# Performance work log

Hardware: AMD Instinct MI355X
Metric: run time of the kernel (lower is better)

## Reference

```python
import jax, jax.numpy as jnp
import numpy as np

B, S, D, H = 4, 2048, 1024, 16
DK = D // H

def setup_inputs() -> dict:
    key = jax.random.key(0)
    ks = jax.random.split(key, 5)
    x = jax.random.normal(ks[0], (B, S, D), dtype=jnp.float32)
    scale = 1.0 / np.sqrt(D)
    Wq = jax.random.normal(ks[1], (D, D), dtype=jnp.float32) * scale
    Wk = jax.random.normal(ks[2], (D, D), dtype=jnp.float32) * scale
    Wv = jax.random.normal(ks[3], (D, D), dtype=jnp.float32) * scale
    Wo = jax.random.normal(ks[4], (D, D), dtype=jnp.float32) * scale
    return {"x": x, "Wq": Wq, "Wk": Wk, "Wv": Wv, "Wo": Wo}

def reference(x, Wq, Wk, Wv, Wo):
    # F.linear: y = x @ W.T  (weights stored torch-style [out, in])
    q = jnp.einsum('bsd,ed->bse', x, Wq).reshape(B, S, H, DK).transpose(0, 2, 1, 3)
    k = jnp.einsum('bsd,ed->bse', x, Wk).reshape(B, S, H, DK).transpose(0, 2, 1, 3)
    v = jnp.einsum('bsd,ed->bse', x, Wv).reshape(B, S, H, DK).transpose(0, 2, 1, 3)
    scores = jnp.einsum('bhqd,bhkd->bhqk', q, k) / jnp.sqrt(jnp.float32(DK))
    attn = jax.nn.softmax(scores, axis=-1)  # dropout p=0.0 -> identity
    out = jnp.einsum('bhqk,bhkd->bhqd', attn, v)
    out = out.transpose(0, 2, 1, 3).reshape(B, S, D)
    return jnp.einsum('bsd,ed->bse', out, Wo)
```

## Files before the change

### kernel.cpp

```cpp
#include <hip/hip_runtime.h>
#include <hip/hip_bf16.h>

#define B_ 4
#define S_ 2048
#define D_ 1024
#define H_ 16
#define DK_ 64

typedef __attribute__((ext_vector_type(8))) short short8;
typedef __attribute__((ext_vector_type(4))) float floatx4;
typedef __attribute__((ext_vector_type(16))) float floatx16;
typedef __attribute__((ext_vector_type(4))) unsigned int uint4v;

#define QSCL 0.1803368801111204f

static __device__ __forceinline__ unsigned short f2bf(float f) {
    unsigned int u = __float_as_uint(f);
    u += 0x7fffu + ((u >> 16) & 1u);
    return (unsigned short)(u >> 16);
}

static __device__ __forceinline__ unsigned int pack2bf_perm(float a, float b) {
    unsigned int u0 = __float_as_uint(a) + 0x8000u;
    unsigned int u1 = __float_as_uint(b) + 0x8000u;
    return __builtin_amdgcn_perm(u1, u0, 0x07060302u);
}

static __device__ __forceinline__ unsigned int pack2bf(float a, float b) {
    return (unsigned int)f2bf(a) | ((unsigned int)f2bf(b) << 16);
}

#define PLSWAP(a, b) asm volatile("v_permlane32_swap_b32 %0, %1" : "+v"(a), "+v"(b))

struct CastAll {
    const float* x;
    const float* w[4];
    unsigned short* xd;
    unsigned short* wd[4];
};

__global__ void cast_all_kernel(CastAll a) {
    int i = blockIdx.x * blockDim.x + threadIdx.x;
    const float* s;
    unsigned short* d;
    int j;
    if (i < 2097152) {
        s = a.x; d = a.xd; j = i;
    } else {
        int k = i - 2097152;
        int w = k >> 18;
        j = k & 262143;
        s = a.w[w]; d = a.wd[w];
    }
    float4 v = ((const float4*)s)[j];
    ushort4 o;
    o.x = f2bf(v.x); o.y = f2bf(v.y); o.z = f2bf(v.z); o.w = f2bf(v.w);
    ((ushort4*)d)[j] = o;
}

template <typename OutT, bool VT2>
__global__ __launch_bounds__(256) void gemm_bt(
    const unsigned short* __restrict__ A,
    const unsigned short* __restrict__ W0,
    const unsigned short* __restrict__ W1,
    const unsigned short* __restrict__ W2,
    OutT* __restrict__ C0, OutT* __restrict__ C1, OutT* __restrict__ C2,
    int M, int N, int K)
{
    __shared__ __align__(16) unsigned short At[128 * 64];
    __shared__ __align__(16) unsigned short Bt[128 * 64];

    const unsigned short* W = (blockIdx.z == 0) ? W0 : ((blockIdx.z == 1) ? W1 : W2);
    OutT* C = (blockIdx.z == 0) ? C0 : ((blockIdx.z == 1) ? C1 : C2);

    const int m0 = blockIdx.x * 128;
    const int n0 = blockIdx.y * 128;
    const int wv = threadIdx.x >> 6;
    const int ln = threadIdx.x & 63;
    const int l31 = ln & 31;
    const int half = ln >> 5;
    const int wm = (wv >> 1) * 64;
    const int wn = (wv & 1) * 64;

    floatx16 acc[2][2];
#pragma unroll
    for (int mt = 0; mt < 2; mt++)
#pragma unroll
        for (int nt = 0; nt < 2; nt++)
#pragma unroll
            for (int e = 0; e < 16; e++) acc[mt][nt][e] = 0.f;

    const int lr = ln >> 3;
    const int lc = (((ln & 7) ^ lr) * 8);
    const int sw = (l31 & 7);

    for (int k0 = 0; k0 < K; k0 += 64) {
        __syncthreads();
#pragma unroll
        for (int c = 0; c < 4; c++) {
            int rowA = wv * 32 + c * 8;
            const unsigned short* gA = A + (size_t)(m0 + rowA + lr) * K + k0 + lc;
            __builtin_amdgcn_global_load_lds(
                (const __attribute__((address_space(1))) void*)gA,
                (__attribute__((address_space(3))) void*)&At[rowA * 64], 16, 0, 0);
            const unsigned short* gB = W + (size_t)(n0 + rowA + lr) * K + k0 + lc;
            __builtin_amdgcn_global_load_lds(
                (const __attribute__((address_space(1))) void*)gB,
                (__attribute__((address_space(3))) void*)&Bt[rowA * 64], 16, 0, 0);
        }
        __syncthreads();

#pragma unroll
        for (int ks = 0; ks < 4; ks++) {
            const int slot = ((ks * 2 + half) ^ sw) * 8;
            short8 af[2], bf[2];
#pragma unroll
            for (int mt = 0; mt < 2; mt++)
                af[mt] = *(const short8*)&At[(wm + mt * 32 + l31) * 64 + slot];
#pragma unroll
            for (int nt = 0; nt < 2; nt++)
                bf[nt] = *(const short8*)&Bt[(wn + nt * 32 + l31) * 64 + slot];
#pragma unroll
            for (int mt = 0; mt < 2; mt++)
#pragma unroll
                for (int nt = 0; nt < 2; nt++)
                    acc[mt][nt] = __builtin_amdgcn_mfma_f32_32x32x16_bf16(af[mt], bf[nt], acc[mt][nt], 0, 0, 0);
        }
    }

    const float esc = (VT2 && blockIdx.z == 0) ? QSCL : 1.0f;

    if constexpr (VT2) {
        if (blockIdx.z == 2) {
            unsigned short* Vt = (unsigned short*)C;
#pragma unroll
            for (int mt = 0; mt < 2; mt++)
#pragma unroll
                for (int nt = 0; nt < 2; nt++)
#pragma unroll
                    for (int rg = 0; rg < 4; rg++) {
                        int col = n0 + wn + nt * 32 + l31;
                        int row0 = m0 + wm + mt * 32 + 4 * half + 8 * rg;
                        int bb = row0 >> 11, ss = row0 & 2047;
                        size_t addr = ((size_t)(bb * 1024 + col)) * 2048 + ss;
                        uint2 pk;
                        pk.x = pack2bf(acc[mt][nt][4 * rg + 0], acc[mt][nt][4 * rg + 1]);
                        pk.y = pack2bf(acc[mt][nt][4 * rg + 2], acc[mt][nt][4 * rg + 3]);
                        *(uint2*)(Vt + addr) = pk;
                    }
            return;
        }
    }

#pragma unroll
    for (int mt = 0; mt < 2; mt++)
#pragma unroll
        for (int nt = 0; nt < 2; nt++)
#pragma unroll
            for (int rg = 0; rg < 4; rg++)
#pragma unroll
                for (int r = 0; r < 4; r++) {
                    int row = m0 + wm + mt * 32 + 4 * half + 8 * rg + r;
                    int col = n0 + wn + nt * 32 + l31;
                    float v = acc[mt][nt][4 * rg + r] * esc;
                    if constexpr (sizeof(OutT) == 2)
                        C[(size_t)row * N + col] = (OutT)f2bf(v);
                    else
                        C[(size_t)row * N + col] = v;
                }
}

__global__ __launch_bounds__(512, 4) void flash_attn(
    const unsigned short* __restrict__ Q,
    const unsigned short* __restrict__ K,
    const unsigned short* __restrict__ Vt,
    unsigned short* __restrict__ O)
{
    __shared__ __align__(16) unsigned short Kt[2][64 * 72];
    __shared__ __align__(16) unsigned short VT[2][64 * 72];

    const int pair = blockIdx.x;
    const int h = pair & 15;
    const int b = pair >> 4;
    const int qt = blockIdx.y;
    const int tid = threadIdx.x;
    const int wv = tid >> 6;
    const int ln = tid & 63;
    const int l31 = ln & 31;
    const int half = ln >> 5;

    const size_t base = ((size_t)b * S_) * D_ + (size_t)h * DK_;
    const size_t vtbase = ((size_t)(b * 1024 + h * 64)) * (size_t)S_;

    const int qrow = qt * 256 + wv * 32 + l31;
    short8 qf[4];
    {
        const unsigned short* qp = Q + base + (size_t)qrow * D_ + half * 8;
#pragma unroll
        for (int ks = 0; ks < 4; ks++) qf[ks] = *(const short8*)(qp + ks * 16);
    }

    floatx16 Oacc[2];
#pragma unroll
    for (int mt = 0; mt < 2; mt++)
#pragma unroll
        for (int e = 0; e < 16; e++) Oacc[mt][e] = 0.f;
    float l_i = 0.f;

    const int srow = tid >> 3;
    const int scol = (tid & 7) * 8;
    const unsigned short* kp = K + base + (size_t)srow * D_ + scol;
    const unsigned short* vp = Vt + vtbase + (size_t)srow * S_ + scol;
    const int swo = srow * 72 + scol;

    short8 kr = *(const short8*)kp;
    short8 vr = *(const short8*)vp;
    kp += (size_t)64 * D_;
    vp += 64;

    for (int kt = 0; kt < S_ / 64; kt++) {
        const int cb = kt & 1;
        unsigned short* Kc = &Kt[cb][0];
        unsigned short* Vc = &VT[cb][0];
        *(short8*)&Kc[swo] = kr;
        *(short8*)&Vc[swo] = vr;
        __syncthreads();

        if (kt < S_ / 64 - 1) {
            kr = *(const short8*)kp;
            vr = *(const short8*)vp;
            kp += (size_t)64 * D_;
            vp += 64;
        }

        uint2 run[2][4];

#pragma unroll
        for (int mt = 0; mt < 2; mt++) {
            floatx16 sac;
#pragma unroll
            for (int e = 0; e < 16; e++) sac[e] = 0.f;
            __builtin_amdgcn_s_setprio(1);
#pragma unroll
            for (int ks = 0; ks < 4; ks++) {
                short8 kf = *(const short8*)&Kc[(mt * 32 + l31) * 72 + ks * 16 + half * 8];
                sac = __builtin_amdgcn_mfma_f32_32x32x16_bf16(kf, qf[ks], sac, 0, 0, 0);
            }
            __builtin_amdgcn_s_setprio(0);
#pragma unroll
            for (int g = 0; g < 4; g++) {
                float p0 = __builtin_amdgcn_exp2f(sac[4 * g + 0]);
                float p1 = __builtin_amdgcn_exp2f(sac[4 * g + 1]);
                float p2 = __builtin_amdgcn_exp2f(sac[4 * g + 2]);
                float p3 = __builtin_amdgcn_exp2f(sac[4 * g + 3]);
                l_i += (p0 + p1) + (p2 + p3);
                run[mt][g].x = pack2bf_perm(p0, p1);
                run[mt][g].y = pack2bf_perm(p2, p3);
            }
        }

#pragma unroll
        for (int mt = 0; mt < 2; mt++)
#pragma unroll
            for (int t = 0; t < 2; t++) {
                PLSWAP(run[mt][2 * t].x, run[mt][2 * t + 1].x);
                PLSWAP(run[mt][2 * t].y, run[mt][2 * t + 1].y);
            }

#pragma unroll
        for (int mt2 = 0; mt2 < 2; mt2++)
#pragma unroll
            for (int t = 0; t < 2; t++) {
                int ks = mt2 * 2 + t;
                uint4v u = {run[mt2][2 * t].x, run[mt2][2 * t].y,
                            run[mt2][2 * t + 1].x, run[mt2][2 * t + 1].y};
                short8 pf = __builtin_bit_cast(short8, u);
                __builtin_amdgcn_s_setprio(1);
#pragma unroll
                for (int mt = 0; mt < 2; mt++) {
                    short8 vf = *(const short8*)&Vc[(mt * 32 + l31) * 72 + ks * 16 + half * 8];
                    Oacc[mt] = __builtin_amdgcn_mfma_f32_32x32x16_bf16(vf, pf, Oacc[mt], 0, 0, 0);
                }
                __builtin_amdgcn_s_setprio(0);
            }
    }

    {
        float ls = l_i + __shfl_xor(l_i, 32);
        float inv = 1.0f / ls;
        const size_t orow = base + (size_t)qrow * D_;
#pragma unroll
        for (int mt = 0; mt < 2; mt++)
#pragma unroll
            for (int g = 0; g < 4; g++) {
                uint2 pk;
                pk.x = pack2bf(Oacc[mt][4 * g + 0] * inv, Oacc[mt][4 * g + 1] * inv);
                pk.y = pack2bf(Oacc[mt][4 * g + 2] * inv, Oacc[mt][4 * g + 3] * inv);
                *(uint2*)(O + orow + mt * 32 + 8 * g + 4 * half) = pk;
            }
    }
}

extern "C" void kernel_launch(void* const* d_in, const int* in_sizes, int n_in,
                              void* d_out, int out_size, void* d_ws, size_t ws_size,
                              hipStream_t stream) {
    const float* x  = (const float*)d_in[0];
    const float* Wq = (const float*)d_in[1];
    const float* Wk = (const float*)d_in[2];
    const float* Wv = (const float*)d_in[3];
    const float* Wo = (const float*)d_in[4];
    float* out = (float*)d_out;

    char* ws = (char*)d_ws;
    const size_t MB = 1024 * 1024;
    unsigned short* xb  = (unsigned short*)(ws);
    unsigned short* wqb = (unsigned short*)(ws + 16 * MB);
    unsigned short* wkb = (unsigned short*)(ws + 18 * MB);
    unsigned short* wvb = (unsigned short*)(ws + 20 * MB);
    unsigned short* wob = (unsigned short*)(ws + 22 * MB);
    unsigned short* Qb  = (unsigned short*)(ws + 24 * MB);
    unsigned short* Kb  = (unsigned short*)(ws + 40 * MB);
    unsigned short* Vtb = (unsigned short*)(ws + 56 * MB);
    unsigned short* Ob  = (unsigned short*)(ws);

    CastAll ca;
    ca.x = x; ca.xd = xb;
    ca.w[0] = Wq; ca.w[1] = Wk; ca.w[2] = Wv; ca.w[3] = Wo;
    ca.wd[0] = wqb; ca.wd[1] = wkb; ca.wd[2] = wvb; ca.wd[3] = wob;
    cast_all_kernel<<<12288, 256, 0, stream>>>(ca);

    dim3 gq((B_ * S_) / 128, D_ / 128, 3);
    gemm_bt<unsigned short, true><<<gq, 256, 0, stream>>>(
        xb, wqb, wkb, wvb, Qb, Kb, Vtb, B_ * S_, D_, D_);

    dim3 gf(64, S_ / 256, 1);
    flash_attn<<<gf, 512, 0, stream>>>(Qb, Kb, Vtb, Ob);

    dim3 go((B_ * S_) / 128, D_ / 128, 1);
    gemm_bt<float, false><<<go, 256, 0, stream>>>(
        Ob, wob, wob, wob, out, out, out, B_ * S_, D_, D_);
}
```

Measured before the change: 269.8 us.

## Fuse Q/K/V projections into one GEMM kernel sharing the A tile

Replaces the three-way z-dimension QKV GEMM launch with a dedicated kernel where each block loads the x tile once and multiplies it against all three weight tiles, keeping three accumulator sets. This cuts redundant global loads of the activation tile and raises MFMA work per LDS load of A. It also raises MFMA priority around the compute loop with s_setprio. The cost is triple accumulator register pressure, which may spill or cap occupancy despite launch_bounds(256,2), plus fewer blocks (512 instead of 1536).

New measurement: 474.8 us. 1.76x slower.

```diff
diff --git a/kernel.cpp b/kernel.cpp
--- a/kernel.cpp
+++ b/kernel.cpp
@@ -58,20 +58,134 @@
     ((ushort4*)d)[j] = o;
 }
 
-template <typename OutT, bool VT2>
+__global__ __launch_bounds__(256, 2) void qkv_gemm(
+    const unsigned short* __restrict__ A,
+    const unsigned short* __restrict__ Wq,
+    const unsigned short* __restrict__ Wk,
+    const unsigned short* __restrict__ Wv,
+    unsigned short* __restrict__ Qo,
+    unsigned short* __restrict__ Ko,
+    unsigned short* __restrict__ Vt)
+{
+    __shared__ __align__(16) unsigned short At[128 * 64];
+    __shared__ __align__(16) unsigned short Bt[3][128 * 64];
+
+    const int m0 = blockIdx.x * 128;
+    const int n0 = blockIdx.y * 128;
+    const int K = D_;
+    const int wv = threadIdx.x >> 6;
+    const int ln = threadIdx.x & 63;
+    const int l31 = ln & 31;
+    const int half = ln >> 5;
+    const int wm = (wv >> 1) * 64;
+    const int wn = (wv & 1) * 64;
+
+    floatx16 acc[3][2][2];
+#pragma unroll
+    for (int w = 0; w < 3; w++)
+#pragma unroll
+        for (int mt = 0; mt < 2; mt++)
+#pragma unroll
+            for (int nt = 0; nt < 2; nt++)
+#pragma unroll
+                for (int e = 0; e < 16; e++) acc[w][mt][nt][e] = 0.f;
+
+    const int lr = ln >> 3;
+    const int lc = (((ln & 7) ^ lr) * 8);
+    const int sw = (l31 & 7);
+
+    for (int k0 = 0; k0 < K; k0 += 64) {
+        __syncthreads();
+#pragma unroll
+        for (int c = 0; c < 4; c++) {
+            const int rowb = wv * 32 + c * 8;
+            const unsigned short* gA = A + (size_t)(m0 + rowb + lr) * K + k0 + lc;
+            __builtin_amdgcn_global_load_lds(
+                (const __attribute__((address_space(1))) void*)gA,
+                (__attribute__((address_space(3))) void*)&At[rowb * 64], 16, 0, 0);
+        }
+#pragma unroll
+        for (int w = 0; w < 3; w++) {
+            const unsigned short* Wsrc = (w == 0) ? Wq : ((w == 1) ? Wk : Wv);
+#pragma unroll
+            for (int c = 0; c < 4; c++) {
+                const int rowb = wv * 32 + c * 8;
+                const unsigned short* gB = Wsrc + (size_t)(n0 + rowb + lr) * K + k0 + lc;
+                __builtin_amdgcn_global_load_lds(
+                    (const __attribute__((address_space(1))) void*)gB,
+                    (__attribute__((address_space(3))) void*)&Bt[w][rowb * 64], 16, 0, 0);
+            }
+        }
+        __syncthreads();
+
+#pragma unroll
+        for (int ks = 0; ks < 4; ks++) {
+            const int slot = ((ks * 2 + half) ^ sw) * 8;
+            short8 af[2];
+#pragma unroll
+            for (int mt = 0; mt < 2; mt++)
+                af[mt] = *(const short8*)&At[(wm + mt * 32 + l31) * 64 + slot];
+            short8 bf[3][2];
+#pragma unroll
+            for (int w = 0; w < 3; w++)
+#pragma unroll
+                for (int nt = 0; nt < 2; nt++)
+                    bf[w][nt] = *(const short8*)&Bt[w][(wn + nt * 32 + l31) * 64 + slot];
+            __builtin_amdgcn_s_setprio(1);
+#pragma unroll
+            for (int w = 0; w < 3; w++)
+#pragma unroll
+                for (int mt = 0; mt < 2; mt++)
+#pragma unroll
+                    for (int nt = 0; nt < 2; nt++)
+                        acc[w][mt][nt] = __builtin_amdgcn_mfma_f32_32x32x16_bf16(
+                            af[mt], bf[w][nt], acc[w][mt][nt], 0, 0, 0);
+            __builtin_amdgcn_s_setprio(0);
+        }
+    }
+
+#pragma unroll
+    for (int w = 0; w < 2; w++) {
+        unsigned short* C = (w == 0) ? Qo : Ko;
+        const float esc = (w == 0) ? QSCL : 1.0f;
+#pragma unroll
+        for (int mt = 0; mt < 2; mt++)
+#pragma unroll
+            for (int nt = 0; nt < 2; nt++)
+#pragma unroll
+                for (int rg = 0; rg < 4; rg++)
+#pragma unroll
+                    for (int r = 0; r < 4; r++) {
+                        int row = m0 + wm + mt * 32 + 4 * half + 8 * rg + r;
+                        int col = n0 + wn + nt * 32 + l31;
+                        C[(size_t)row * D_ + col] = f2bf(acc[w][mt][nt][4 * rg + r] * esc);
+                    }
+    }
+#pragma unroll
+    for (int mt = 0; mt < 2; mt++)
+#pragma unroll
+        for (int nt = 0; nt < 2; nt++)
+#pragma unroll
+            for (int rg = 0; rg < 4; rg++) {
+                int col = n0 + wn + nt * 32 + l31;
+                int row0 = m0 + wm + mt * 32 + 4 * half + 8 * rg;
+                int bb = row0 >> 11, ss = row0 & 2047;
+                size_t addr = ((size_t)(bb * 1024 + col)) * 2048 + ss;
+                uint2 pk;
+                pk.x = pack2bf(acc[2][mt][nt][4 * rg + 0], acc[2][mt][nt][4 * rg + 1]);
+                pk.y = pack2bf(acc[2][mt][nt][4 * rg + 2], acc[2][mt][nt][4 * rg + 3]);
+                *(uint2*)(Vt + addr) = pk;
+            }
+}
+
 __global__ __launch_bounds__(256) void gemm_bt(
     const unsigned short* __restrict__ A,
-    const unsigned short* __restrict__ W0,
-    const unsigned short* __restrict__ W1,
-    const unsigned short* __restrict__ W2,
-    OutT* __restrict__ C0, OutT* __restrict__ C1, OutT* __restrict__ C2,
+    const unsigned short* __restrict__ W,
+    float* __restrict__ C,
     int M, int N, int K)
 {
     __shared__ __align__(16) unsigned short At[128 * 64];
     __shared__ __align__(16) unsigned short Bt[128 * 64];
-
-    const unsigned short* W = (blockIdx.z == 0) ? W0 : ((blockIdx.z == 1) ? W1 : W2);
-    OutT* C = (blockIdx.z == 0) ? C0 : ((blockIdx.z == 1) ? C1 : C2);
 
     const int m0 = blockIdx.x * 128;
     const int n0 = blockIdx.y * 128;
@@ -128,30 +242,6 @@
         }
     }
 
-    const float esc = (VT2 && blockIdx.z == 0) ? QSCL : 1.0f;
-
-    if constexpr (VT2) {
-        if (blockIdx.z == 2) {
-            unsigned short* Vt = (unsigned short*)C;
-#pragma unroll
-            for (int mt = 0; mt < 2; mt++)
-#pragma unroll
-                for (int nt = 0; nt < 2; nt++)
-#pragma unroll
-                    for (int rg = 0; rg < 4; rg++) {
-                        int col = n0 + wn + nt * 32 + l31;
-                        int row0 = m0 + wm + mt * 32 + 4 * half + 8 * rg;
-                        int bb = row0 >> 11, ss = row0 & 2047;
-                        size_t addr = ((size_t)(bb * 1024 + col)) * 2048 + ss;
-                        uint2 pk;
-                        pk.x = pack2bf(acc[mt][nt][4 * rg + 0], acc[mt][nt][4 * rg + 1]);
-                        pk.y = pack2bf(acc[mt][nt][4 * rg + 2], acc[mt][nt][4 * rg + 3]);
-                        *(uint2*)(Vt + addr) = pk;
-                    }
-            return;
-        }
-    }
-
 #pragma unroll
     for (int mt = 0; mt < 2; mt++)
 #pragma unroll
@@ -162,11 +252,7 @@
                 for (int r = 0; r < 4; r++) {
                     int row = m0 + wm + mt * 32 + 4 * half + 8 * rg + r;
                     int col = n0 + wn + nt * 32 + l31;
-                    float v = acc[mt][nt][4 * rg + r] * esc;
-                    if constexpr (sizeof(OutT) == 2)
-                        C[(size_t)row * N + col] = (OutT)f2bf(v);
-                    else
-                        C[(size_t)row * N + col] = v;
+                    C[(size_t)row * N + col] = acc[mt][nt][4 * rg + r];
                 }
 }
 
@@ -329,14 +415,12 @@
     ca.wd[0] = wqb; ca.wd[1] = wkb; ca.wd[2] = wvb; ca.wd[3] = wob;
     cast_all_kernel<<<12288, 256, 0, stream>>>(ca);
 
-    dim3 gq((B_ * S_) / 128, D_ / 128, 3);
-    gemm_bt<unsigned short, true><<<gq, 256, 0, stream>>>(
-        xb, wqb, wkb, wvb, Qb, Kb, Vtb, B_ * S_, D_, D_);
+    dim3 gq((B_ * S_) / 128, D_ / 128, 1);
+    qkv_gemm<<<gq, 256, 0, stream>>>(xb, wqb, wkb, wvb, Qb, Kb, Vtb);
 
     dim3 gf(64, S_ / 256, 1);
     flash_attn<<<gf, 512, 0, stream>>>(Qb, Kb, Vtb, Ob);
 
     dim3 go((B_ * S_) / 128, D_ / 128, 1);
-    gemm_bt<float, false><<<go, 256, 0, stream>>>(
-        Ob, wob, wob, wob, out, out, out, B_ * S_, D_, D_);
-}
+    gemm_bt<<<go, 256, 0, stream>>>(Ob, wob, out, B_ * S_, D_, D_);
+}
```
